# Kernel optimization log

Hardware: AMD Instinct MI355X
Metric: run time of the kernel (lower is better)

Reference implementation:

```python
import jax, jax.numpy as jnp
import numpy as np

B, S, E, H, D = 4, 2048, 1024, 16, 64


def setup_inputs() -> dict:
    key = jax.random.key(0)
    ks = jax.random.split(key, 6)
    scale_in = 1.0 / np.sqrt(E)
    return {
        "x": jax.random.normal(ks[0], (B, S, E), dtype=jnp.float32),
        "Wq": jax.random.normal(ks[1], (H, E, D), dtype=jnp.float32) * scale_in,
        "bq": jnp.zeros((H, D), dtype=jnp.float32),
        "Wk": jax.random.normal(ks[2], (H, E, D), dtype=jnp.float32) * scale_in,
        "bk": jnp.zeros((H, D), dtype=jnp.float32),
        "Wv": jax.random.normal(ks[3], (H, E, D), dtype=jnp.float32) * scale_in,
        "bv": jnp.zeros((H, D), dtype=jnp.float32),
        "Wo": jax.random.normal(ks[4], (H * D, E), dtype=jnp.float32) * (1.0 / np.sqrt(H * D)),
        "bo": jnp.zeros((E,), dtype=jnp.float32),
    }


def reference(x, Wq, bq, Wk, bk, Wv, bv, Wo, bo):
    # Per-head Q/K/V projections, batched over heads: [B,S,E] x [H,E,D] -> [B,H,S,D]
    q = jnp.einsum("bse,hed->bhsd", x, Wq) + bq[None, :, None, :]
    k = jnp.einsum("bse,hed->bhsd", x, Wk) + bk[None, :, None, :]
    v = jnp.einsum("bse,hed->bhsd", x, Wv) + bv[None, :, None, :]

    d = q.shape[-1]
    scores = jnp.einsum("bhqd,bhkd->bhqk", q, k) / jnp.sqrt(jnp.asarray(d, q.dtype))
    # Causal mask (registered tril buffer of size max_seq_len in HeadAttention)
    seq = scores.shape[-1]
    causal = jnp.tril(jnp.ones((seq, seq), dtype=bool))
    scores = jnp.where(causal[None, None, :, :], scores, jnp.asarray(-1e9, scores.dtype))
    attn = jax.nn.softmax(scores, axis=-1)
    out = jnp.einsum("bhqk,bhkd->bhqd", attn, v)  # [B,H,S,D]

    # Concat heads: [B,S,H*D], then output projection (dropout is identity in eval)
    out = out.transpose(0, 2, 1, 3).reshape(out.shape[0], out.shape[2], -1)
    return out @ Wo + bo
```

## Files before the change

### kernel.cpp

```cpp
#include <hip/hip_runtime.h>

typedef __bf16 bf16x8 __attribute__((ext_vector_type(8)));
typedef __bf16 bf16x4 __attribute__((ext_vector_type(4)));
typedef float  f32x4  __attribute__((ext_vector_type(4)));

#define B_    4
#define S_    2048
#define E_    1024
#define H_    16
#define D_    64
#define MROWS (B_*S_)
#define HD3   3072

#define SCORE_SCALE 0.18033688011112043f

__device__ __forceinline__ void load_lds16(const void* g, void* l) {
  __builtin_amdgcn_global_load_lds((__attribute__((address_space(1))) void*)g,
                                   (__attribute__((address_space(3))) void*)l,
                                   16, 0, 0);
}

__device__ __forceinline__ f32x4 mfma16(bf16x8 a, bf16x8 b, f32x4 c) {
  return __builtin_amdgcn_mfma_f32_16x16x32_bf16(a, b, c, 0, 0, 0);
}

__device__ __forceinline__ int swz(int row, int dchunk) {
  return row * 64 + ((dchunk ^ (row & 7)) * 8);
}


__global__ void prep(const float4* __restrict__ x, const float* __restrict__ Wq,
                     const float* __restrict__ Wk, const float* __restrict__ Wv,
                     const float* __restrict__ bq, const float* __restrict__ bk,
                     const float* __restrict__ bv, const float* __restrict__ Wo,
                     __bf16* __restrict__ xb, __bf16* __restrict__ Wt,
                     float* __restrict__ bqkv, __bf16* __restrict__ Wot) {
  __shared__ float t[64][65];
  int bid = blockIdx.x;
  if (bid < 8192) {
    int id = bid * 256 + threadIdx.x;
    float4 v = x[id];
    bf16x4 o = { (__bf16)v.x, (__bf16)v.y, (__bf16)v.z, (__bf16)v.w };
    *(bf16x4*)(xb + 4 * (size_t)id) = o;
    return;
  }
  int tx = threadIdx.x & 63;
  int ty = threadIdx.x >> 6;
  if (bid < 8960) {
    int b2 = bid - 8192;
    int e0 = (b2 & 15) * 64;
    int h  = (b2 >> 4) & 15;
    int p  = b2 >> 8;
    const float* W    = (p == 0) ? Wq : (p == 1) ? Wk : Wv;
    const float* bsrc = (p == 0) ? bq : (p == 1) ? bk : bv;
#pragma unroll
    for (int r = 0; r < 16; ++r) {
      int eL = ty + r * 4;
      t[eL][tx] = W[((size_t)h * 1024 + (e0 + eL)) * 64 + tx];
    }
    __syncthreads();
#pragma unroll
    for (int r = 0; r < 16; ++r) {
      int d = ty + r * 4;
      Wt[((size_t)(p * 1024 + h * 64 + d)) * 1024 + e0 + tx] = (__bf16)t[tx][d];
    }
    if ((b2 & 15) == 0 && threadIdx.x < 64)
      bqkv[p * 1024 + h * 64 + threadIdx.x] = bsrc[h * 64 + threadIdx.x];
  } else {
    int b2 = bid - 8960;
    int hd0 = (b2 >> 4) * 64;
    int e0  = (b2 & 15) * 64;
#pragma unroll
    for (int r = 0; r < 16; ++r) {
      int hdL = ty + r * 4;
      t[hdL][tx] = Wo[(size_t)(hd0 + hdL) * 1024 + e0 + tx];
    }
    __syncthreads();
#pragma unroll
    for (int r = 0; r < 16; ++r) {
      int eL = ty + r * 4;
      Wot[(size_t)(e0 + eL) * 1024 + hd0 + tx] = (__bf16)t[tx][eL];
    }
  }
}

__global__ void vt_pack(const __bf16* __restrict__ QKV, __bf16* __restrict__ VT) {
  __shared__ __attribute__((aligned(16))) __bf16 t[64 * 80];
  int bx = blockIdx.x;
  int st = bx & 31, bh = bx >> 5;
  int b = bh >> 4, h = bh & 15;
  int s0 = st * 64;
  const __bf16* src = QKV + ((size_t)(b * S_ + s0)) * HD3 + 2048 + h * 64;
  int tid = threadIdx.x;
#pragma unroll
  for (int p = 0; p < 2; ++p) {
    int g = tid + p * 256;
    int s = g >> 3, ch = g & 7;
    bf16x8 v = *(const bf16x8*)(src + (size_t)s * HD3 + ch * 8);
    *(bf16x8*)&t[s * 80 + ch * 8] = v;
  }
  __syncthreads();
#pragma unroll
  for (int p = 0; p < 2; ++p) {
    int g = tid + p * 256;
    int d = g >> 3, sc = g & 7;
    bf16x8 v;
#pragma unroll
    for (int u = 0; u < 8; ++u) v[u] = t[(sc * 8 + u) * 80 + d];
    *(bf16x8*)&VT[((size_t)(bh * 64 + d)) * 2048 + s0 + sc * 8] = v;
  }
}


template <int STORE_BF16, int QSCALE>
__global__ __launch_bounds__(256) void gemm_bt(const __bf16* __restrict__ A,
                                               const __bf16* __restrict__ Bt,
                                               const float* __restrict__ bias,
                                               void* __restrict__ Cout,
                                               int M, int N, int K) {
  __shared__ __attribute__((aligned(16))) __bf16 As[128 * 64];
  __shared__ __attribute__((aligned(16))) __bf16 Bs[128 * 64];
  int tid = threadIdx.x, wave = tid >> 6, lane = tid & 63;
  int quad = lane >> 4, cc = lane & 15;
  int nb = N >> 7;
  int bm = (int)blockIdx.x / nb, bn = (int)blockIdx.x % nb;
  const __bf16* Abase = A + (size_t)bm * 128 * K;
  const __bf16* Bbase = Bt + (size_t)bn * 128 * K;
  int wr = (wave >> 1) * 64, wc = (wave & 1) * 64;
  f32x4 acc[4][4];
#pragma unroll
  for (int i = 0; i < 4; ++i)
#pragma unroll
    for (int j = 0; j < 4; ++j) acc[i][j] = (f32x4){0.f, 0.f, 0.f, 0.f};

  for (int k0 = 0; k0 < K; k0 += 64) {
    __syncthreads();
#pragma unroll
    for (int p = 0; p < 4; ++p) {
      int g = tid + p * 256;
      int row = g >> 3, pch = g & 7;
      int gcol = k0 + ((pch ^ (row & 7)) * 8);
      load_lds16(Abase + (size_t)row * K + gcol, &As[g * 8]);
      load_lds16(Bbase + (size_t)row * K + gcol, &Bs[g * 8]);
    }
    __syncthreads();
#pragma unroll
    for (int kk = 0; kk < 2; ++kk) {
      bf16x8 af[4], bf[4];
#pragma unroll
      for (int i = 0; i < 4; ++i) af[i] = *(const bf16x8*)&As[swz(wr + i * 16 + cc, kk * 4 + quad)];
#pragma unroll
      for (int j = 0; j < 4; ++j) bf[j] = *(const bf16x8*)&Bs[swz(wc + j * 16 + cc, kk * 4 + quad)];
#pragma unroll
      for (int i = 0; i < 4; ++i)
#pragma unroll
        for (int j = 0; j < 4; ++j) acc[i][j] = mfma16(af[i], bf[j], acc[i][j]);
    }
  }
#pragma unroll
  for (int j = 0; j < 4; ++j) {
    int col = bn * 128 + wc + j * 16 + cc;
    float bv = bias[col];
    float sc = (QSCALE && col < 1024) ? SCORE_SCALE : 1.0f;
#pragma unroll
    for (int i = 0; i < 4; ++i) {
      int row0 = bm * 128 + wr + i * 16 + quad * 4;
#pragma unroll
      for (int r = 0; r < 4; ++r) {
        float v = (acc[i][j][r] + bv) * sc;
        if (STORE_BF16) ((__bf16*)Cout)[(size_t)(row0 + r) * N + col] = (__bf16)v;
        else            ((float*)Cout)[(size_t)(row0 + r) * N + col] = v;
      }
    }
  }
}


__global__ __launch_bounds__(256, 3) void attn(const __bf16* __restrict__ QKV,
                                               const __bf16* __restrict__ VT,
                                               __bf16* __restrict__ O) {
  int bx = blockIdx.x;
  int bh = bx & 63;
  int qt = 15 - (bx >> 6);
  int h  = bh & 15;
  int b  = bh >> 4;
  int q0 = qt * 128;
  int tid = threadIdx.x, wave = tid >> 6, lane = tid & 63;
  int quad = lane >> 4, c = lane & 15;

  __shared__ __attribute__((aligned(16))) __bf16 smem[24576];
  __bf16* Qs = smem;
  __bf16* Ks = smem + 8192;
  __bf16* Vs = smem + 16384;
  __bf16* Ps = smem + wave * 2048;

  const __bf16* Qbase = QKV + (size_t)(b * S_ + q0) * HD3 + h * 64;
  const __bf16* Vbase = VT + (size_t)bh * (64 * 2048);
#pragma unroll
  for (int p = 0; p < 4; ++p) {
    int g = tid + p * 256;
    int row = g >> 3, pch = g & 7;
    load_lds16(Qbase + (size_t)row * HD3 + (pch ^ (row & 7)) * 8, &Qs[g * 8]);
  }
  {
    const __bf16* Kb = QKV + (size_t)(b * S_) * HD3 + 1024 + h * 64;
#pragma unroll
    for (int p = 0; p < 2; ++p) {
      int g = tid + p * 256;
      int row = g >> 3, pch = g & 7;
      load_lds16(Kb + (size_t)row * HD3 + (pch ^ (row & 7)) * 8, &Ks[g * 8]);
      load_lds16(Vbase + (size_t)row * 2048 + (pch ^ (row & 7)) * 8, &Vs[g * 8]);
    }
  }
  __syncthreads();

  bf16x8 qf[2][2];
#pragma unroll
  for (int i = 0; i < 2; ++i)
#pragma unroll
    for (int kk = 0; kk < 2; ++kk)
      qf[i][kk] = *(const bf16x8*)&Qs[swz(wave * 32 + i * 16 + c, kk * 4 + quad)];

  const __bf16 one_b = (__bf16)1.0f;
  bf16x8 ones = { one_b, one_b, one_b, one_b, one_b, one_b, one_b, one_b };

  f32x4 acc_o[2][4], acc_l[2];
#pragma unroll
  for (int i = 0; i < 2; ++i) {
    acc_l[i] = (f32x4){0.f, 0.f, 0.f, 0.f};
#pragma unroll
    for (int j = 0; j < 4; ++j) acc_o[i][j] = (f32x4){0.f, 0.f, 0.f, 0.f};
  }

  int ntiles = qt * 2 + 2;
  for (int t = 0; t < ntiles; ++t) {
    int cur = t & 1;
    if (t + 1 < ntiles) {
      int kv1 = (t + 1) * 64;
      const __bf16* Kb = QKV + (size_t)(b * S_ + kv1) * HD3 + 1024 + h * 64;
      const __bf16* Vb = Vbase + kv1;
      __bf16* Kd = Ks + (cur ^ 1) * 4096;
      __bf16* Vd = Vs + (cur ^ 1) * 4096;
#pragma unroll
      for (int p = 0; p < 2; ++p) {
        int g = tid + p * 256;
        int row = g >> 3, pch = g & 7;
        load_lds16(Kb + (size_t)row * HD3 + (pch ^ (row & 7)) * 8, &Kd[g * 8]);
        load_lds16(Vb + (size_t)row * 2048 + (pch ^ (row & 7)) * 8, &Vd[g * 8]);
      }
    }

    const __bf16* Kc = Ks + cur * 4096;
    const __bf16* Vc = Vs + cur * 4096;

    f32x4 acc_t[2][4];
#pragma unroll
    for (int i = 0; i < 2; ++i)
#pragma unroll
      for (int j = 0; j < 4; ++j) acc_t[i][j] = (f32x4){0.f, 0.f, 0.f, 0.f};
    bf16x8 kf[4][2];
#pragma unroll
    for (int j = 0; j < 4; ++j)
#pragma unroll
      for (int kk = 0; kk < 2; ++kk)
        kf[j][kk] = *(const bf16x8*)&Kc[swz(j * 16 + c, kk * 4 + quad)];
#pragma unroll
    for (int i = 0; i < 2; ++i)
#pragma unroll
      for (int j = 0; j < 4; ++j)
#pragma unroll
        for (int kk = 0; kk < 2; ++kk)
          acc_t[i][j] = mfma16(kf[j][kk], qf[i][kk], acc_t[i][j]);

    bool domask = (t >= ntiles - 2);
    int kv0 = t * 64;
#pragma unroll
    for (int i = 0; i < 2; ++i) {
      int q_l = i * 16 + c;
      int q_g = q0 + wave * 32 + q_l;
#pragma unroll
      for (int j = 0; j < 4; ++j) {
        bf16x4 pk;
#pragma unroll
        for (int r = 0; r < 4; ++r) {
          float p = __builtin_amdgcn_exp2f(acc_t[i][j][r]);
          if (domask) {
            int kv = kv0 + j * 16 + quad * 4 + r;
            p = (kv > q_g) ? 0.f : p;
          }
          pk[r] = (__bf16)p;
        }
        int dch8 = j * 2 + (quad >> 1);
        int phys = q_l * 64 + ((dch8 ^ (q_l & 7)) * 8) + (quad & 1) * 4;
        *(bf16x4*)&Ps[phys] = pk;
      }
    }

    bf16x8 pf[2][2], vf[4][2];
#pragma unroll
    for (int i = 0; i < 2; ++i)
#pragma unroll
      for (int kk = 0; kk < 2; ++kk)
        pf[i][kk] = *(const bf16x8*)&Ps[swz(i * 16 + c, kk * 4 + quad)];
#pragma unroll
    for (int j = 0; j < 4; ++j)
#pragma unroll
      for (int kk = 0; kk < 2; ++kk)
        vf[j][kk] = *(const bf16x8*)&Vc[swz(j * 16 + c, kk * 4 + quad)];
#pragma unroll
    for (int i = 0; i < 2; ++i) {
#pragma unroll
      for (int j = 0; j < 4; ++j)
#pragma unroll
        for (int kk = 0; kk < 2; ++kk)
          acc_o[i][j] = mfma16(pf[i][kk], vf[j][kk], acc_o[i][j]);
      acc_l[i] = mfma16(pf[i][0], ones, acc_l[i]);
      acc_l[i] = mfma16(pf[i][1], ones, acc_l[i]);
    }

    __syncthreads();
  }

  __bf16* Obase = O + (size_t)(b * S_ + q0) * 1024 + h * 64;
#pragma unroll
  for (int i = 0; i < 2; ++i)
#pragma unroll
    for (int r = 0; r < 4; ++r) {
      float rl = 1.0f / acc_l[i][r];
      int row = wave * 32 + i * 16 + quad * 4 + r;
#pragma unroll
      for (int j = 0; j < 4; ++j)
        Obase[(size_t)row * 1024 + j * 16 + c] = (__bf16)(acc_o[i][j][r] * rl);
    }
}


extern "C" void kernel_launch(void* const* d_in, const int* in_sizes, int n_in,
                              void* d_out, int out_size, void* d_ws, size_t ws_size,
                              hipStream_t stream) {
  (void)in_sizes; (void)n_in; (void)out_size; (void)ws_size;
  const float* x  = (const float*)d_in[0];
  const float* Wq = (const float*)d_in[1];
  const float* bq = (const float*)d_in[2];
  const float* Wk = (const float*)d_in[3];
  const float* bk = (const float*)d_in[4];
  const float* Wv = (const float*)d_in[5];
  const float* bv = (const float*)d_in[6];
  const float* Wo = (const float*)d_in[7];
  const float* bo = (const float*)d_in[8];

  char* w = (char*)d_ws;
  __bf16* xb   = (__bf16*)(w);
  __bf16* Wt   = (__bf16*)(w + (16ull << 20));
  __bf16* Wot  = (__bf16*)(w + (22ull << 20));
  float*  bqkv = (float*) (w + (24ull << 20));
  __bf16* QKVb = (__bf16*)(w + (25ull << 20));
  __bf16* Ob   = (__bf16*)(w + (73ull << 20));
  __bf16* VT   = (__bf16*)(w + (89ull << 20));

  prep   <<<9216, 256, 0, stream>>>((const float4*)x, Wq, Wk, Wv, bq, bk, bv, Wo,
                                    xb, Wt, bqkv, Wot);
  gemm_bt<1,1><<<dim3((MROWS / 128) * (3072 / 128)), 256, 0, stream>>>(xb, Wt, bqkv, (void*)QKVb, MROWS, 3072, 1024);
  vt_pack<<<2048, 256, 0, stream>>>(QKVb, VT);
  attn   <<<1024, 256, 0, stream>>>(QKVb, VT, Ob);
  gemm_bt<0,0><<<dim3((MROWS / 128) * (1024 / 128)), 256, 0, stream>>>(Ob, Wot, bo, d_out, MROWS, 1024, 1024);
}
```

Baseline: 259.8 us.

## Double attention query tile to 256 rows with 8 waves per block

The attention kernel now runs 512-thread blocks covering 256 query rows, so each K/V tile loaded into shared memory is reused by 8 waves instead of 4, halving K/V global traffic per query. Waves skip compute on KV tiles entirely above their causal diagonal, and masking is decided per wave. The block order is changed to interleave heavy and light query tiles, which is meant to balance load. The grid shrinks to 512 blocks, which lowers parallelism, and waves near the start of a block sit idle through barriers while their block mates work on later tiles.

```diff
diff --git a/kernel.cpp b/kernel.cpp
--- a/kernel.cpp
+++ b/kernel.cpp
@@ -176,41 +176,37 @@
 }
 
 
-__global__ __launch_bounds__(256, 3) void attn(const __bf16* __restrict__ QKV,
+__global__ __launch_bounds__(512, 4) void attn(const __bf16* __restrict__ QKV,
                                                const __bf16* __restrict__ VT,
                                                __bf16* __restrict__ O) {
   int bx = blockIdx.x;
   int bh = bx & 63;
-  int qt = 15 - (bx >> 6);
+  int qt = (bx < 256) ? (7 - (bx >> 6)) : ((bx >> 6) - 4);
   int h  = bh & 15;
   int b  = bh >> 4;
-  int q0 = qt * 128;
+  int q0 = qt * 256;
   int tid = threadIdx.x, wave = tid >> 6, lane = tid & 63;
   int quad = lane >> 4, c = lane & 15;
 
-  __shared__ __attribute__((aligned(16))) __bf16 smem[24576];
+  __shared__ __attribute__((aligned(16))) __bf16 smem[32768];
   __bf16* Qs = smem;
-  __bf16* Ks = smem + 8192;
-  __bf16* Vs = smem + 16384;
+  __bf16* Ks = smem + 16384;
+  __bf16* Vs = smem + 24576;
   __bf16* Ps = smem + wave * 2048;
 
   const __bf16* Qbase = QKV + (size_t)(b * S_ + q0) * HD3 + h * 64;
   const __bf16* Vbase = VT + (size_t)bh * (64 * 2048);
 #pragma unroll
   for (int p = 0; p < 4; ++p) {
-    int g = tid + p * 256;
+    int g = tid + p * 512;
     int row = g >> 3, pch = g & 7;
     load_lds16(Qbase + (size_t)row * HD3 + (pch ^ (row & 7)) * 8, &Qs[g * 8]);
   }
   {
     const __bf16* Kb = QKV + (size_t)(b * S_) * HD3 + 1024 + h * 64;
-#pragma unroll
-    for (int p = 0; p < 2; ++p) {
-      int g = tid + p * 256;
-      int row = g >> 3, pch = g & 7;
-      load_lds16(Kb + (size_t)row * HD3 + (pch ^ (row & 7)) * 8, &Ks[g * 8]);
-      load_lds16(Vbase + (size_t)row * 2048 + (pch ^ (row & 7)) * 8, &Vs[g * 8]);
-    }
+    int row = tid >> 3, pch = tid & 7;
+    load_lds16(Kb + (size_t)row * HD3 + (pch ^ (row & 7)) * 8, &Ks[tid * 8]);
+    load_lds16(Vbase + (size_t)row * 2048 + (pch ^ (row & 7)) * 8, &Vs[tid * 8]);
   }
   __syncthreads();
 
@@ -232,90 +228,89 @@
     for (int j = 0; j < 4; ++j) acc_o[i][j] = (f32x4){0.f, 0.f, 0.f, 0.f};
   }
 
-  int ntiles = qt * 2 + 2;
+  int qwave = q0 + wave * 32;
+  int ntiles = qt * 4 + 4;
   for (int t = 0; t < ntiles; ++t) {
     int cur = t & 1;
     if (t + 1 < ntiles) {
       int kv1 = (t + 1) * 64;
       const __bf16* Kb = QKV + (size_t)(b * S_ + kv1) * HD3 + 1024 + h * 64;
       const __bf16* Vb = Vbase + kv1;
-      __bf16* Kd = Ks + (cur ^ 1) * 4096;
-      __bf16* Vd = Vs + (cur ^ 1) * 4096;
-#pragma unroll
-      for (int p = 0; p < 2; ++p) {
-        int g = tid + p * 256;
-        int row = g >> 3, pch = g & 7;
-        load_lds16(Kb + (size_t)row * HD3 + (pch ^ (row & 7)) * 8, &Kd[g * 8]);
-        load_lds16(Vb + (size_t)row * 2048 + (pch ^ (row & 7)) * 8, &Vd[g * 8]);
+      int row = tid >> 3, pch = tid & 7;
+      load_lds16(Kb + (size_t)row * HD3 + (pch ^ (row & 7)) * 8,
+                 &Ks[(cur ^ 1) * 4096 + tid * 8]);
+      load_lds16(Vb + (size_t)row * 2048 + (pch ^ (row & 7)) * 8,
+                 &Vs[(cur ^ 1) * 4096 + tid * 8]);
+    }
+
+    int kv0 = t * 64;
+    if (kv0 <= qwave + 31) {
+      const __bf16* Kc = Ks + cur * 4096;
+      const __bf16* Vc = Vs + cur * 4096;
+
+      f32x4 acc_t[2][4];
+#pragma unroll
+      for (int i = 0; i < 2; ++i)
+#pragma unroll
+        for (int j = 0; j < 4; ++j) acc_t[i][j] = (f32x4){0.f, 0.f, 0.f, 0.f};
+      bf16x8 kf[4][2];
+#pragma unroll
+      for (int j = 0; j < 4; ++j)
+#pragma unroll
+        for (int kk = 0; kk < 2; ++kk)
+          kf[j][kk] = *(const bf16x8*)&Kc[swz(j * 16 + c, kk * 4 + quad)];
+#pragma unroll
+      for (int i = 0; i < 2; ++i)
+#pragma unroll
+        for (int j = 0; j < 4; ++j)
+#pragma unroll
+          for (int kk = 0; kk < 2; ++kk)
+            acc_t[i][j] = mfma16(kf[j][kk], qf[i][kk], acc_t[i][j]);
+
+      bool domask = (kv0 + 63 > qwave);
+#pragma unroll
+      for (int i = 0; i < 2; ++i) {
+        int q_l = i * 16 + c;
+        int q_g = qwave + q_l;
+#pragma unroll
+        for (int j = 0; j < 4; ++j) {
+          bf16x4 pk;
+#pragma unroll
+          for (int r = 0; r < 4; ++r) {
+            float p = __builtin_amdgcn_exp2f(acc_t[i][j][r]);
+            if (domask) {
+              int kv = kv0 + j * 16 + quad * 4 + r;
+              p = (kv > q_g) ? 0.f : p;
+            }
+            pk[r] = (__bf16)p;
+          }
+          int dch8 = j * 2 + (quad >> 1);
+          int phys = q_l * 64 + ((dch8 ^ (q_l & 7)) * 8) + (quad & 1) * 4;
+          *(bf16x4*)&Ps[phys] = pk;
+        }
       }
-    }
-
-    const __bf16* Kc = Ks + cur * 4096;
-    const __bf16* Vc = Vs + cur * 4096;
-
-    f32x4 acc_t[2][4];
-#pragma unroll
-    for (int i = 0; i < 2; ++i)
-#pragma unroll
-      for (int j = 0; j < 4; ++j) acc_t[i][j] = (f32x4){0.f, 0.f, 0.f, 0.f};
-    bf16x8 kf[4][2];
-#pragma unroll
-    for (int j = 0; j < 4; ++j)
-#pragma unroll
-      for (int kk = 0; kk < 2; ++kk)
-        kf[j][kk] = *(const bf16x8*)&Kc[swz(j * 16 + c, kk * 4 + quad)];
-#pragma unroll
-    for (int i = 0; i < 2; ++i)
+
+      bf16x8 pf[2][2], vf[4][2];
+#pragma unroll
+      for (int i = 0; i < 2; ++i)
+#pragma unroll
+        for (int kk = 0; kk < 2; ++kk)
+          pf[i][kk] = *(const bf16x8*)&Ps[swz(i * 16 + c, kk * 4 + quad)];
 #pragma unroll
       for (int j = 0; j < 4; ++j)
 #pragma unroll
         for (int kk = 0; kk < 2; ++kk)
-          acc_t[i][j] = mfma16(kf[j][kk], qf[i][kk], acc_t[i][j]);
-
-    bool domask = (t >= ntiles - 2);
-    int kv0 = t * 64;
-#pragma unroll
-    for (int i = 0; i < 2; ++i) {
-      int q_l = i * 16 + c;
-      int q_g = q0 + wave * 32 + q_l;
-#pragma unroll
-      for (int j = 0; j < 4; ++j) {
-        bf16x4 pk;
-#pragma unroll
-        for (int r = 0; r < 4; ++r) {
-          float p = __builtin_amdgcn_exp2f(acc_t[i][j][r]);
-          if (domask) {
-            int kv = kv0 + j * 16 + quad * 4 + r;
-            p = (kv > q_g) ? 0.f : p;
-          }
-          pk[r] = (__bf16)p;
-        }
-        int dch8 = j * 2 + (quad >> 1);
-        int phys = q_l * 64 + ((dch8 ^ (q_l & 7)) * 8) + (quad & 1) * 4;
-        *(bf16x4*)&Ps[phys] = pk;
+          vf[j][kk] = *(const bf16x8*)&Vc[swz(j * 16 + c, kk * 4 + quad)];
+#pragma unroll
+      for (int i = 0; i < 2; ++i) {
+#pragma unroll
+        for (int j = 0; j < 4; ++j)
+#pragma unroll
+          for (int kk = 0; kk < 2; ++kk)
+            acc_o[i][j] = mfma16(pf[i][kk], vf[j][kk], acc_o[i][j]);
+        acc_l[i] = mfma16(pf[i][0], ones, acc_l[i]);
+        acc_l[i] = mfma16(pf[i][1], ones, acc_l[i]);
       }
-    }
-
-    bf16x8 pf[2][2], vf[4][2];
-#pragma unroll
-    for (int i = 0; i < 2; ++i)
-#pragma unroll
-      for (int kk = 0; kk < 2; ++kk)
-        pf[i][kk] = *(const bf16x8*)&Ps[swz(i * 16 + c, kk * 4 + quad)];
-#pragma unroll
-    for (int j = 0; j < 4; ++j)
-#pragma unroll
-      for (int kk = 0; kk < 2; ++kk)
-        vf[j][kk] = *(const bf16x8*)&Vc[swz(j * 16 + c, kk * 4 + quad)];
-#pragma unroll
-    for (int i = 0; i < 2; ++i) {
-#pragma unroll
-      for (int j = 0; j < 4; ++j)
-#pragma unroll
-        for (int kk = 0; kk < 2; ++kk)
-          acc_o[i][j] = mfma16(pf[i][kk], vf[j][kk], acc_o[i][j]);
-      acc_l[i] = mfma16(pf[i][0], ones, acc_l[i]);
-      acc_l[i] = mfma16(pf[i][1], ones, acc_l[i]);
     }
 
     __syncthreads();
@@ -362,6 +357,6 @@
                                     xb, Wt, bqkv, Wot);
   gemm_bt<1,1><<<dim3((MROWS / 128) * (3072 / 128)), 256, 0, stream>>>(xb, Wt, bqkv, (void*)QKVb, MROWS, 3072, 1024);
   vt_pack<<<2048, 256, 0, stream>>>(QKVb, VT);
-  attn   <<<1024, 256, 0, stream>>>(QKVb, VT, Ob);
+  attn   <<<512, 512, 0, stream>>>(QKVb, VT, Ob);
   gemm_bt<0,0><<<dim3((MROWS / 128) * (1024 / 128)), 256, 0, stream>>>(Ob, Wot, bo, d_out, MROWS, 1024, 1024);
 }
```

Measured after the change: 255.7 us. About the same (-1.6%).
